# Performance work log

Hardware: AMD Instinct MI355X
Metric: run time of the kernel (lower is better)

## Reference

```python
import jax, jax.numpy as jnp
import numpy as np
from jax.scipy.special import logsumexp

B, DK, N, M = 16, 512, 1024, 1024
SINKHORN_ITERS = 5
EPS = 1e-8


def setup_inputs() -> dict:
    key = jax.random.key(0)
    k1, k2, k3, k4, k5 = jax.random.split(key, 5)
    return {
        "src_embedding": jax.random.normal(k1, (B, DK, N), dtype=jnp.float32),
        "tgt_embedding": jax.random.normal(k2, (B, DK, M), dtype=jnp.float32),
        "src": jax.random.normal(k3, (B, 3, N), dtype=jnp.float32),
        "tgt": jax.random.normal(k4, (B, 3, M), dtype=jnp.float32),
        # temperature must be positive; uniform in [0.05, 1.0)
        "temperature": jax.random.uniform(k5, (B,), dtype=jnp.float32, minval=0.05, maxval=1.0),
    }


def sinkhorn(scores, n_iters):
    # ZeroPad2d((0,1,0,1)): pad one slack row and one slack column with zeros
    scores = jnp.pad(scores, ((0, 0), (0, 1), (0, 1)))
    for _ in range(n_iters):
        # row normalization (all rows except slack row)
        top = scores[:, :-1, :] - logsumexp(scores[:, :-1, :], axis=2, keepdims=True)
        scores = jnp.concatenate([top, scores[:, -1:, :]], axis=1)
        # column normalization (all cols except slack col)
        left = scores[:, :, :-1] - logsumexp(scores[:, :, :-1], axis=1, keepdims=True)
        scores = jnp.concatenate([left, scores[:, :, -1:]], axis=2)
    return scores[:, :-1, :-1]


def reference(src_embedding, tgt_embedding, src, tgt, temperature):
    b, d_k, n = src_embedding.shape
    # [B, N, M] similarity scores
    dists = jnp.einsum('bdn,bdm->bnm', src_embedding, tgt_embedding) / jnp.sqrt(jnp.float32(d_k))
    affinity = dists / temperature[:, None, None]
    log_perm = sinkhorn(affinity, SINKHORN_ITERS)
    perm = jnp.exp(log_perm)                                             # [B,N,M]
    perm_norm = perm / (jnp.sum(perm, axis=2, keepdims=True) + EPS)      # [B,N,M]
    # soft correspondence: weighted_tgt[b,:,i] = sum_j perm_norm[b,i,j] * tgt[b,:,j]
    weighted_tgt = jnp.einsum('bdm,bnm->bdn', tgt, perm_norm)            # [B,3,N]
    weights = jnp.sum(perm, axis=-1, keepdims=True)                      # [B,N,1]
    weights_norm = weights / (jnp.sum(weights, axis=1, keepdims=True) + EPS)
    weights_norm = jnp.swapaxes(weights_norm, 1, 2)                      # [B,1,N]
    src_centroid = jnp.sum(src * weights_norm, axis=2, keepdims=True)    # [B,3,1]
    tgt_centroid = jnp.sum(weighted_tgt * weights_norm, axis=2, keepdims=True)
    src_centered = src - src_centroid
    corr_centered = (weighted_tgt - tgt_centroid) * weights_norm
    # weighted cross-covariance, batched 3x3
    H = jnp.einsum('bin,bjn->bij', src_centered, corr_centered)          # [B,3,3]
    # batched Procrustes via SVD (torch.svd: H = u diag(s) v^T; jnp: H = u diag(s) vh)
    u, s, vh = jnp.linalg.svd(H)
    v = jnp.swapaxes(vh, 1, 2)
    ut = jnp.swapaxes(u, 1, 2)
    r = jnp.matmul(v, ut)
    r_det = jnp.linalg.det(r)                                            # [B]
    diag = jnp.stack([jnp.ones_like(r_det), jnp.ones_like(r_det), r_det], axis=-1)  # [B,3]
    R = jnp.matmul(v * diag[:, None, :], ut)                             # [B,3,3]
    t = (jnp.matmul(-R, src_centroid) + tgt_centroid).reshape(b, 3)
    return R, t, perm_norm
```

## Files before the change

### kernel.cpp

```cpp
#include <hip/hip_runtime.h>
#include <math.h>

#define BB 16
#define NN 1024
#define MM 1024
#define DKK 512
#define RBLK 16
#define NRB  (NN/RBLK)

typedef short short8 __attribute__((ext_vector_type(8)));
typedef float f32x4 __attribute__((ext_vector_type(4)));

__device__ float g_u[BB*NN];
__device__ float g_v[BB*MM];
__device__ float g_w[BB*NN];
__device__ float g_wt[BB*3*NN];
__device__ float g_pm[BB*NRB*MM];
__device__ float g_ps[BB*NRB*MM];
__device__ __attribute__((aligned(16))) unsigned short gAh[BB*NN*DKK];
__device__ __attribute__((aligned(16))) unsigned short gAl[BB*NN*DKK];
__device__ __attribute__((aligned(16))) unsigned short gBh[BB*MM*DKK];
__device__ __attribute__((aligned(16))) unsigned short gBl[BB*MM*DKK];

__global__ __launch_bounds__(256) void zero_v_kernel() {
    int i = blockIdx.x*256 + threadIdx.x;
    if (i < BB*MM) g_v[i] = 0.0f;
}

__device__ __forceinline__ unsigned int bf16_rne(float x){
    unsigned int u = __float_as_uint(x);
    return (u + 0x7fffu + ((u>>16)&1u)) >> 16;
}

__global__ __launch_bounds__(256) void convert_split(const float* __restrict__ X,
                                                     int which) {
    unsigned short* Hh = which ? gBh : gAh;
    unsigned short* Hl = which ? gBl : gAl;
    int b  = blockIdx.z;
    int d0 = blockIdx.y * 64;
    int i0 = blockIdx.x * 64;
    __shared__ float T[64*65];
    const float* Xb = X + ((size_t)b*DKK + d0)*NN + i0;
    int t = threadIdx.x;
#pragma unroll
    for (int it=0; it<4; ++it){
        int lin = t + 256*it;
        int d = lin >> 4;
        int i4 = lin & 15;
        float4 v = *(const float4*)(Xb + (size_t)d*NN + i4*4);
        T[(i4*4+0)*65 + d] = v.x;
        T[(i4*4+1)*65 + d] = v.y;
        T[(i4*4+2)*65 + d] = v.z;
        T[(i4*4+3)*65 + d] = v.w;
    }
    __syncthreads();
    size_t obase = ((size_t)b*NN + i0)*DKK + d0;
#pragma unroll
    for (int it=0; it<2; ++it){
        int c = t + 256*it;
        int i = c >> 3;
        int p = c & 7;
        unsigned int hw[4], lw[4];
#pragma unroll
        for (int j=0;j<4;j++){
            float x0 = T[i*65 + p*8 + 2*j];
            float x1 = T[i*65 + p*8 + 2*j+1];
            unsigned int h0 = bf16_rne(x0);
            unsigned int h1 = bf16_rne(x1);
            float hf0 = __uint_as_float(h0<<16);
            float hf1 = __uint_as_float(h1<<16);
            unsigned int l0 = bf16_rne(x0 - hf0);
            unsigned int l1 = bf16_rne(x1 - hf1);
            hw[j] = h0 | (h1<<16);
            lw[j] = l0 | (l1<<16);
        }
        size_t eo = obase + (size_t)i*DKK + p*8;
        uint4 hv; hv.x=hw[0]; hv.y=hw[1]; hv.z=hw[2]; hv.w=hw[3];
        uint4 lv; lv.x=lw[0]; lv.y=lw[1]; lv.z=lw[2]; lv.w=lw[3];
        *(uint4*)(Hh + eo) = hv;
        *(uint4*)(Hl + eo) = lv;
    }
}

__global__ __launch_bounds__(256) void gemm_mfma(const float* __restrict__ temp,
                                                 float* __restrict__ C) {
    int id   = blockIdx.x;
    int xcd  = id & 7;
    int slot = id >> 3;
    int b    = xcd*2 + (slot >> 6);
    int sub  = slot & 63;
    int i0   = (sub >> 3) << 7;
    int j0   = (sub & 7) << 7;
    __shared__ __attribute__((aligned(16))) char lds[40960];
    int t = threadIdx.x;
    int lane = t & 63, w = t >> 6;
    int wr = w >> 1, wc = w & 1;
    const size_t eb = (size_t)b * NN * DKK;
    const uint4* pAh = (const uint4*)(gAh + eb);
    const uint4* pAl = (const uint4*)(gAl + eb);
    const uint4* pBh = (const uint4*)(gBh + eb);
    const uint4* pBl = (const uint4*)(gBl + eb);
    int rr = t >> 2, pp = t & 3;

    f32x4 acc[16];
#pragma unroll
    for (int q=0;q<16;q++) acc[q] = (f32x4){0.f,0.f,0.f,0.f};

    uint4 ra0, ra1, la0, la1, rb0, rb1, lb0, lb1;
    auto loadk = [&](int k0){
        int kq = k0 >> 3;
        ra0 = pAh[(size_t)(i0+rr)*64 + kq + pp];
        ra1 = pAh[(size_t)(i0+rr+64)*64 + kq + pp];
        la0 = pAl[(size_t)(i0+rr)*64 + kq + pp];
        la1 = pAl[(size_t)(i0+rr+64)*64 + kq + pp];
        rb0 = pBh[(size_t)(j0+rr)*64 + kq + pp];
        rb1 = pBh[(size_t)(j0+rr+64)*64 + kq + pp];
        lb0 = pBl[(size_t)(j0+rr)*64 + kq + pp];
        lb1 = pBl[(size_t)(j0+rr+64)*64 + kq + pp];
    };
    loadk(0);

    const char* fa = lds + (wr*64 + (lane&15))*80 + (lane>>4)*16;
    const char* fb = lds + 20480 + (wc*64 + (lane&15))*80 + (lane>>4)*16;
    char* wbase = lds + rr*80 + pp*16;

    for (int ks=0; ks<16; ++ks){
        __syncthreads();
        *(uint4*)(wbase + 0)     = ra0;
        *(uint4*)(wbase + 5120)  = ra1;
        *(uint4*)(wbase + 10240) = la0;
        *(uint4*)(wbase + 15360) = la1;
        *(uint4*)(wbase + 20480) = rb0;
        *(uint4*)(wbase + 25600) = rb1;
        *(uint4*)(wbase + 30720) = lb0;
        *(uint4*)(wbase + 35840) = lb1;
        __syncthreads();
        if (ks+1 < 16) loadk((ks+1)*32);

        short8 ah[4], al[4];
#pragma unroll
        for (int mf=0;mf<4;mf++){
            ah[mf] = *(const short8*)(fa + mf*1280);
            al[mf] = *(const short8*)(fa + 10240 + mf*1280);
        }
#pragma unroll
        for (int nf=0;nf<4;nf++){
            short8 bh = *(const short8*)(fb + nf*1280);
            short8 bl = *(const short8*)(fb + 10240 + nf*1280);
#pragma unroll
            for (int mf=0;mf<4;mf++){
                acc[mf*4+nf] = __builtin_amdgcn_mfma_f32_16x16x32_bf16(ah[mf], bh, acc[mf*4+nf], 0,0,0);
                acc[mf*4+nf] = __builtin_amdgcn_mfma_f32_16x16x32_bf16(ah[mf], bl, acc[mf*4+nf], 0,0,0);
                acc[mf*4+nf] = __builtin_amdgcn_mfma_f32_16x16x32_bf16(al[mf], bh, acc[mf*4+nf], 0,0,0);
            }
        }
    }

    float scale = 1.0f/(22.62741699796952f * temp[b]);
    float* Cb = C + ((size_t)b<<20);
    int r0c = i0 + wr*64 + ((lane>>4)<<2);
    int c0c = j0 + wc*64 + (lane&15);
#pragma unroll
    for (int mf=0;mf<4;mf++){
#pragma unroll
        for (int r2=0;r2<4;r2++){
            float* rowp = Cb + (size_t)(r0c + mf*16 + r2)*MM + c0c;
#pragma unroll
            for (int nf=0;nf<4;nf++)
                rowp[nf*16] = acc[mf*4+nf][r2]*scale;
        }
    }
}

__global__ __launch_bounds__(256) void sink_iter(const float* __restrict__ S) {
    int b   = blockIdx.y;
    int rb  = blockIdx.x;
    int row0 = rb*RBLK;
    int t = threadIdx.x;
    __shared__ float Ls[RBLK*1028];
    __shared__ float v_l[1024];
    __shared__ float u_l[RBLK];

    float4 v4 = *(const float4*)(g_v + (b<<10) + t*4);
    *(float4*)(v_l + t*4) = v4;

    const float* Sb = S + ((size_t)b*NN + row0)*MM;
#pragma unroll
    for (int rr=0; rr<RBLK; ++rr){
        float4 s4 = *(const float4*)(Sb + (size_t)rr*MM + t*4);
        s4.x -= v4.x; s4.y -= v4.y; s4.z -= v4.z; s4.w -= v4.w;
        *(float4*)(&Ls[rr*1028 + t*4]) = s4;
    }
    __syncthreads();

    {
        int r = t >> 4, c = t & 15;
        const float* Lr = &Ls[r*1028 + c];
        float m = -INFINITY;
#pragma unroll
        for (int k=0;k<64;k++) m = fmaxf(m, Lr[16*k]);
#pragma unroll
        for (int off=1; off<16; off<<=1) m = fmaxf(m, __shfl_xor(m, off));
        m = fmaxf(m, 0.0f);
        float s = 0.0f;
#pragma unroll
        for (int k=0;k<64;k++) s += __expf(Lr[16*k] - m);
#pragma unroll
        for (int off=1; off<16; off<<=1) s += __shfl_xor(s, off);
        s += __expf(-m);
        float u = m + __logf(s);
        if (c==0){ u_l[r] = u; g_u[b*NN + row0 + r] = u; }
    }
    __syncthreads();

    float mm[4], ss[4];
#pragma unroll
    for (int q=0;q<4;q++){ mm[q]=-INFINITY; ss[q]=0.f; }
#pragma unroll
    for (int r=0;r<RBLK;++r){
        float ur = u_l[r];
        const float* Lr = &Ls[r*1028];
#pragma unroll
        for (int q=0;q<4;q++)
            mm[q] = fmaxf(mm[q], Lr[t + 256*q] - ur);
    }
#pragma unroll
    for (int r=0;r<RBLK;++r){
        float ur = u_l[r];
        const float* Lr = &Ls[r*1028];
#pragma unroll
        for (int q=0;q<4;q++)
            ss[q] += __expf(Lr[t + 256*q] - ur - mm[q]);
    }
    size_t pbase = ((size_t)(b*NRB + rb) << 10) + t;
#pragma unroll
    for (int q=0;q<4;q++){
        g_pm[pbase + 256*q] = mm[q] + v_l[t + 256*q];
        g_ps[pbase + 256*q] = ss[q];
    }
}

__global__ __launch_bounds__(256) void col_lse_combine() {
    int idx = blockIdx.x*256 + threadIdx.x;
    int b = idx >> 10; int j = idx & (MM-1);
    float m = -INFINITY, s = 0.0f;
    size_t base = ((size_t)(b*NRB) << 10) + j;
    for (int c=0;c<NRB;c++){
        float om = g_pm[base + ((size_t)c<<10)];
        float os = g_ps[base + ((size_t)c<<10)];
        float nm = fmaxf(m, om);
        s = s*__expf(m-nm) + os*__expf(om-nm);
        m = nm;
    }
    float nm = fmaxf(m, 0.0f);
    s = s*__expf(m-nm) + __expf(-nm);
    g_v[idx] = nm + __logf(s);
}

__global__ __launch_bounds__(256) void finalize_rows(float* __restrict__ S,
                                                     const float* __restrict__ tgt) {
    int row  = blockIdx.x*4 + (threadIdx.x>>6);
    int lane = threadIdx.x & 63;
    int b = row >> 10;
    int i = row & (NN-1);
    float ui = g_u[row];
    float4* srow = (float4*)(S + (size_t)row*MM);
    const float4* vb = (const float4*)(g_v + (b<<10));
    const float4* t0 = (const float4*)(tgt + (size_t)b*3*MM);
    const float4* t1 = (const float4*)(tgt + (size_t)b*3*MM + MM);
    const float4* t2 = (const float4*)(tgt + (size_t)b*3*MM + 2*MM);
    float p[16];
    float rs=0.f, a0=0.f, a1=0.f, a2=0.f;
#pragma unroll
    for (int k=0;k<4;k++){
        float4 s4 = srow[lane + 64*k];
        float4 v4 = vb[lane + 64*k];
        p[4*k+0] = __expf(s4.x - ui - v4.x);
        p[4*k+1] = __expf(s4.y - ui - v4.y);
        p[4*k+2] = __expf(s4.z - ui - v4.z);
        p[4*k+3] = __expf(s4.w - ui - v4.w);
        rs += p[4*k+0]+p[4*k+1]+p[4*k+2]+p[4*k+3];
        float4 w0 = t0[lane + 64*k];
        float4 w1 = t1[lane + 64*k];
        float4 w2 = t2[lane + 64*k];
        a0 += p[4*k+0]*w0.x + p[4*k+1]*w0.y + p[4*k+2]*w0.z + p[4*k+3]*w0.w;
        a1 += p[4*k+0]*w1.x + p[4*k+1]*w1.y + p[4*k+2]*w1.z + p[4*k+3]*w1.w;
        a2 += p[4*k+0]*w2.x + p[4*k+1]*w2.y + p[4*k+2]*w2.z + p[4*k+3]*w2.w;
    }
    for (int off=32; off; off>>=1){
        rs += __shfl_xor(rs, off);
        a0 += __shfl_xor(a0, off);
        a1 += __shfl_xor(a1, off);
        a2 += __shfl_xor(a2, off);
    }
    float inv = 1.0f/(rs + 1e-8f);
#pragma unroll
    for (int k=0;k<4;k++){
        srow[lane + 64*k] = make_float4(p[4*k+0]*inv, p[4*k+1]*inv, p[4*k+2]*inv, p[4*k+3]*inv);
    }
    if (lane==0){
        g_w[row] = rs;
        g_wt[(b*3+0)*NN + i] = a0*inv;
        g_wt[(b*3+1)*NN + i] = a1*inv;
        g_wt[(b*3+2)*NN + i] = a2*inv;
    }
}

__global__ __launch_bounds__(256) void procrustes(const float* __restrict__ src,
                                                  float* __restrict__ out) {
    int b = blockIdx.x;
    int t = threadIdx.x;
    __shared__ float red[256];
    auto bsum = [&](float v)->float{
        red[t]=v; __syncthreads();
        for (int o=128;o>0;o>>=1){ if(t<o) red[t]+=red[t+o]; __syncthreads(); }
        float r=red[0]; __syncthreads(); return r;
    };
    const float* wrow = g_w + b*NN;
    float pw=0.f;
    for (int i=t;i<NN;i+=256) pw += wrow[i];
    float W = bsum(pw);
    float winv = 1.0f/(W + 1e-8f);
    const float* sb  = src  + (size_t)b*3*NN;
    const float* wtb = g_wt + (size_t)b*3*NN;
    float sc[3], tc[3];
    for (int c=0;c<3;c++){
        float p1=0.f,p2=0.f;
        for (int i=t;i<NN;i+=256){
            float wn = wrow[i]*winv;
            p1 += sb[c*NN+i]*wn;
            p2 += wtb[c*NN+i]*wn;
        }
        sc[c]=bsum(p1);
        tc[c]=bsum(p2);
    }
    float H[9];
    for (int c=0;c<3;c++)
        for (int d=0;d<3;d++){
            float p=0.f;
            for (int i=t;i<NN;i+=256){
                float wn = wrow[i]*winv;
                p += (sb[c*NN+i]-sc[c]) * ((wtb[d*NN+i]-tc[d])*wn);
            }
            H[c*3+d]=bsum(p);
        }
    if (t==0){
        double Hd[3][3];
        for (int r2=0;r2<3;r2++) for (int c2=0;c2<3;c2++) Hd[r2][c2]=H[r2*3+c2];
        double K[3][3];
        for (int i2=0;i2<3;i2++)
            for (int j2=0;j2<3;j2++){
                double acc=0;
                for (int r2=0;r2<3;r2++) acc += Hd[r2][i2]*Hd[r2][j2];
                K[i2][j2]=acc;
            }
        double V[3][3]={{1,0,0},{0,1,0},{0,0,1}};
        const int PQ[3][2]={{0,1},{0,2},{1,2}};
        for (int sweep=0; sweep<30; ++sweep){
            double off = fabs(K[0][1])+fabs(K[0][2])+fabs(K[1][2]);
            if (off < 1e-26) break;
            for (int pi=0; pi<3; ++pi){
                int p = PQ[pi][0], q = PQ[pi][1];
                double apq = K[p][q];
                if (fabs(apq) < 1e-300) continue;
                double tau = (K[q][q]-K[p][p])/(2.0*apq);
                double tt  = (tau>=0.0?1.0:-1.0)/(fabs(tau)+sqrt(1.0+tau*tau));
                double c   = 1.0/sqrt(1.0+tt*tt);
                double s   = tt*c;
                double Kpp=K[p][p], Kqq=K[q][q];
                K[p][p] = Kpp - tt*apq;
                K[q][q] = Kqq + tt*apq;
                K[p][q] = 0.0; K[q][p] = 0.0;
                int r2 = 3-p-q;
                double Krp=K[r2][p], Krq=K[r2][q];
                K[r2][p] = c*Krp - s*Krq; K[p][r2]=K[r2][p];
                K[r2][q] = s*Krp + c*Krq; K[q][r2]=K[r2][q];
                for (int rr=0; rr<3; ++rr){
                    double vp=V[rr][p], vq=V[rr][q];
                    V[rr][p] = c*vp - s*vq;
                    V[rr][q] = s*vp + c*vq;
                }
            }
        }
        double lam[3]={K[0][0],K[1][1],K[2][2]};
        int o0=0,o1=1,o2=2,tmp;
        if (lam[o0]<lam[o1]){tmp=o0;o0=o1;o1=tmp;}
        if (lam[o0]<lam[o2]){tmp=o0;o0=o2;o2=tmp;}
        if (lam[o1]<lam[o2]){tmp=o1;o1=o2;o2=tmp;}
        int ord[3]={o0,o1,o2};
        double Vs[3][3], U[3][3];
        for (int k=0;k<3;k++)
            for (int r2=0;r2<3;r2++) Vs[r2][k]=V[r2][ord[k]];
        for (int k=0;k<3;k++){
            double ux = Hd[0][0]*Vs[0][k] + Hd[0][1]*Vs[1][k] + Hd[0][2]*Vs[2][k];
            double uy = Hd[1][0]*Vs[0][k] + Hd[1][1]*Vs[1][k] + Hd[1][2]*Vs[2][k];
            double uz = Hd[2][0]*Vs[0][k] + Hd[2][1]*Vs[1][k] + Hd[2][2]*Vs[2][k];
            double n = sqrt(ux*ux+uy*uy+uz*uz);
            if (n > 1e-30){ U[0][k]=ux/n; U[1][k]=uy/n; U[2][k]=uz/n; }
            else {
                double cx = U[1][0]*U[2][1]-U[2][0]*U[1][1];
                double cy = U[2][0]*U[0][1]-U[0][0]*U[2][1];
                double cz = U[0][0]*U[1][1]-U[1][0]*U[0][1];
                U[0][k]=cx; U[1][k]=cy; U[2][k]=cz;
            }
        }
        double rm[3][3];
        for (int i2=0;i2<3;i2++)
            for (int j2=0;j2<3;j2++)
                rm[i2][j2] = Vs[i2][0]*U[j2][0] + Vs[i2][1]*U[j2][1] + Vs[i2][2]*U[j2][2];
        double det = rm[0][0]*(rm[1][1]*rm[2][2]-rm[1][2]*rm[2][1])
                   - rm[0][1]*(rm[1][0]*rm[2][2]-rm[1][2]*rm[2][0])
                   + rm[0][2]*(rm[1][0]*rm[2][1]-rm[1][1]*rm[2][0]);
        double R[3][3];
        for (int i2=0;i2<3;i2++)
            for (int j2=0;j2<3;j2++)
                R[i2][j2] = Vs[i2][0]*U[j2][0] + Vs[i2][1]*U[j2][1] + det*Vs[i2][2]*U[j2][2];
        double tv[3];
        for (int i2=0;i2<3;i2++)
            tv[i2] = -(R[i2][0]*sc[0]+R[i2][1]*sc[1]+R[i2][2]*sc[2]) + tc[i2];
        for (int i2=0;i2<3;i2++)
            for (int j2=0;j2<3;j2++)
                out[b*9 + i2*3 + j2] = (float)R[i2][j2];
        for (int i2=0;i2<3;i2++)
            out[144 + b*3 + i2] = (float)tv[i2];
    }
}

extern "C" void kernel_launch(void* const* d_in, const int* in_sizes, int n_in,
                              void* d_out, int out_size, void* d_ws, size_t ws_size,
                              hipStream_t stream) {
    const float* src_emb = (const float*)d_in[0];
    const float* tgt_emb = (const float*)d_in[1];
    const float* src     = (const float*)d_in[2];
    const float* tgt     = (const float*)d_in[3];
    const float* temp    = (const float*)d_in[4];
    float* out = (float*)d_out;
    float* S = out + 192;

    hipLaunchKernelGGL(zero_v_kernel, dim3(64), dim3(256), 0, stream);
    hipLaunchKernelGGL(convert_split, dim3(16,8,16), dim3(256), 0, stream, src_emb, 0);
    hipLaunchKernelGGL(convert_split, dim3(16,8,16), dim3(256), 0, stream, tgt_emb, 1);
    hipLaunchKernelGGL(gemm_mfma, dim3(1024), dim3(256), 0, stream, temp, S);
    for (int it=0; it<5; ++it){
        hipLaunchKernelGGL(sink_iter, dim3(NRB,BB), dim3(256), 0, stream, S);
        hipLaunchKernelGGL(col_lse_combine, dim3(64), dim3(256), 0, stream);
    }
    hipLaunchKernelGGL(finalize_rows, dim3(4096), dim3(256), 0, stream, S, tgt);
    hipLaunchKernelGGL(procrustes, dim3(16), dim3(256), 0, stream, src, out);
}
```

Before: 366.1 us.

## Use direct global-to-LDS loads with double buffering and swizzled layout in split-bf16 GEMM

The GEMM main loop now uses global_load_lds to copy the hi/lo bf16 tiles straight into a double-buffered 64KB LDS region. This removes the register staging, the padded-row stores and one barrier per k-step. The conversion kernel writes a swizzled k-chunk order so the unpadded LDS reads avoid bank conflicts, and the two conversion launches are merged into one grid. The MFMA loop is reordered into three passes over hi/lo fragments, which lowers register pressure. The larger LDS footprint may reduce occupancy, and the swizzle must match exactly between producer and consumer.

```diff
diff --git a/kernel.cpp b/kernel.cpp
--- a/kernel.cpp
+++ b/kernel.cpp
@@ -32,11 +32,20 @@
     return (u + 0x7fffu + ((u>>16)&1u)) >> 16;
 }
 
-__global__ __launch_bounds__(256) void convert_split(const float* __restrict__ X,
-                                                     int which) {
+__device__ __forceinline__ void gl_lds(const void* g, void* l){
+    __builtin_amdgcn_global_load_lds(
+        (const __attribute__((address_space(1))) unsigned int*)g,
+        (__attribute__((address_space(3))) unsigned int*)l, 16, 0, 0);
+}
+
+__global__ __launch_bounds__(256) void convert_split(const float* __restrict__ A,
+                                                     const float* __restrict__ Bm) {
+    int z = blockIdx.z;
+    int which = z >> 4;
+    int b = z & 15;
+    const float* X = which ? Bm : A;
     unsigned short* Hh = which ? gBh : gAh;
     unsigned short* Hl = which ? gBl : gAl;
-    int b  = blockIdx.z;
     int d0 = blockIdx.y * 64;
     int i0 = blockIdx.x * 64;
     __shared__ float T[64*65];
@@ -74,7 +83,8 @@
             hw[j] = h0 | (h1<<16);
             lw[j] = l0 | (l1<<16);
         }
-        size_t eo = obase + (size_t)i*DKK + p*8;
+        int pw = (p & 4) | ((p + (i>>1)) & 3);
+        size_t eo = obase + (size_t)i*DKK + pw*8;
         uint4 hv; hv.x=hw[0]; hv.y=hw[1]; hv.z=hw[2]; hv.w=hw[3];
         uint4 lv; lv.x=lw[0]; lv.y=lw[1]; lv.z=lw[2]; lv.w=lw[3];
         *(uint4*)(Hh + eo) = hv;
@@ -91,69 +101,85 @@
     int sub  = slot & 63;
     int i0   = (sub >> 3) << 7;
     int j0   = (sub & 7) << 7;
-    __shared__ __attribute__((aligned(16))) char lds[40960];
+    __shared__ __attribute__((aligned(16))) char lds[65536];
     int t = threadIdx.x;
     int lane = t & 63, w = t >> 6;
     int wr = w >> 1, wc = w & 1;
-    const size_t eb = (size_t)b * NN * DKK;
-    const uint4* pAh = (const uint4*)(gAh + eb);
-    const uint4* pAl = (const uint4*)(gAl + eb);
-    const uint4* pBh = (const uint4*)(gBh + eb);
-    const uint4* pBl = (const uint4*)(gBl + eb);
-    int rr = t >> 2, pp = t & 3;
+    const size_t ebytes = (size_t)b * NN * DKK * 2;
+
+    const char* src[8];
+    int dstoff[8];
+    {
+        int rql = lane >> 2, cl = lane & 3;
+#pragma unroll
+        for (int o=0;o<4;o++){
+            const char* g = (o==0) ? (const char*)gAh : (o==1) ? (const char*)gAl
+                           : (o==2) ? (const char*)gBh : (const char*)gBl;
+            int t0 = (o<2) ? i0 : j0;
+#pragma unroll
+            for (int q=0;q<2;q++){
+                int rloc = w*32 + q*16 + rql;
+                src[o*2+q] = g + ebytes + (size_t)(t0 + rloc)*1024 + cl*16;
+                dstoff[o*2+q] = o*8192 + (w*32 + q*16)*64;
+            }
+        }
+    }
 
     f32x4 acc[16];
 #pragma unroll
     for (int q=0;q<16;q++) acc[q] = (f32x4){0.f,0.f,0.f,0.f};
 
-    uint4 ra0, ra1, la0, la1, rb0, rb1, lb0, lb1;
-    auto loadk = [&](int k0){
-        int kq = k0 >> 3;
-        ra0 = pAh[(size_t)(i0+rr)*64 + kq + pp];
-        ra1 = pAh[(size_t)(i0+rr+64)*64 + kq + pp];
-        la0 = pAl[(size_t)(i0+rr)*64 + kq + pp];
-        la1 = pAl[(size_t)(i0+rr+64)*64 + kq + pp];
-        rb0 = pBh[(size_t)(j0+rr)*64 + kq + pp];
-        rb1 = pBh[(size_t)(j0+rr+64)*64 + kq + pp];
-        lb0 = pBl[(size_t)(j0+rr)*64 + kq + pp];
-        lb1 = pBl[(size_t)(j0+rr+64)*64 + kq + pp];
-    };
-    loadk(0);
-
-    const char* fa = lds + (wr*64 + (lane&15))*80 + (lane>>4)*16;
-    const char* fb = lds + 20480 + (wc*64 + (lane&15))*80 + (lane>>4)*16;
-    char* wbase = lds + rr*80 + pp*16;
+    int fslot = ((lane>>4) + ((lane&15)>>1)) & 3;
+    int arow = wr*64 + (lane&15);
+    int brow = wc*64 + (lane&15);
+    int faoff = arow*64 + fslot*16;
+    int fboff = 16384 + brow*64 + fslot*16;
+
+#pragma unroll
+    for (int idx=0;idx<8;idx++) gl_lds(src[idx], lds + dstoff[idx]);
 
     for (int ks=0; ks<16; ++ks){
         __syncthreads();
-        *(uint4*)(wbase + 0)     = ra0;
-        *(uint4*)(wbase + 5120)  = ra1;
-        *(uint4*)(wbase + 10240) = la0;
-        *(uint4*)(wbase + 15360) = la1;
-        *(uint4*)(wbase + 20480) = rb0;
-        *(uint4*)(wbase + 25600) = rb1;
-        *(uint4*)(wbase + 30720) = lb0;
-        *(uint4*)(wbase + 35840) = lb1;
-        __syncthreads();
-        if (ks+1 < 16) loadk((ks+1)*32);
-
-        short8 ah[4], al[4];
-#pragma unroll
-        for (int mf=0;mf<4;mf++){
-            ah[mf] = *(const short8*)(fa + mf*1280);
-            al[mf] = *(const short8*)(fa + 10240 + mf*1280);
-        }
-#pragma unroll
-        for (int nf=0;nf<4;nf++){
-            short8 bh = *(const short8*)(fb + nf*1280);
-            short8 bl = *(const short8*)(fb + 10240 + nf*1280);
-#pragma unroll
-            for (int mf=0;mf<4;mf++){
-                acc[mf*4+nf] = __builtin_amdgcn_mfma_f32_16x16x32_bf16(ah[mf], bh, acc[mf*4+nf], 0,0,0);
-                acc[mf*4+nf] = __builtin_amdgcn_mfma_f32_16x16x32_bf16(ah[mf], bl, acc[mf*4+nf], 0,0,0);
-                acc[mf*4+nf] = __builtin_amdgcn_mfma_f32_16x16x32_bf16(al[mf], bh, acc[mf*4+nf], 0,0,0);
-            }
-        }
+        int cur = (ks & 1) * 32768;
+        if (ks+1 < 16){
+            int nxt = ((ks+1) & 1) * 32768;
+#pragma unroll
+            for (int idx=0;idx<8;idx++){
+                src[idx] += 64;
+                gl_lds(src[idx], lds + nxt + dstoff[idx]);
+            }
+        }
+        const char* fa = lds + cur + faoff;
+        const char* fb = lds + cur + fboff;
+
+        short8 ah[4], bh[4];
+#pragma unroll
+        for (int mf=0;mf<4;mf++) ah[mf] = *(const short8*)(fa + mf*1024);
+#pragma unroll
+        for (int nf=0;nf<4;nf++) bh[nf] = *(const short8*)(fb + nf*1024);
+#pragma unroll
+        for (int nf=0;nf<4;nf++)
+#pragma unroll
+            for (int mf=0;mf<4;mf++)
+                acc[mf*4+nf] = __builtin_amdgcn_mfma_f32_16x16x32_bf16(ah[mf], bh[nf], acc[mf*4+nf], 0,0,0);
+
+        short8 al[4];
+#pragma unroll
+        for (int mf=0;mf<4;mf++) al[mf] = *(const short8*)(fa + 8192 + mf*1024);
+#pragma unroll
+        for (int nf=0;nf<4;nf++)
+#pragma unroll
+            for (int mf=0;mf<4;mf++)
+                acc[mf*4+nf] = __builtin_amdgcn_mfma_f32_16x16x32_bf16(al[mf], bh[nf], acc[mf*4+nf], 0,0,0);
+
+        short8 bl[4];
+#pragma unroll
+        for (int nf=0;nf<4;nf++) bl[nf] = *(const short8*)(fb + 8192 + nf*1024);
+#pragma unroll
+        for (int nf=0;nf<4;nf++)
+#pragma unroll
+            for (int mf=0;mf<4;mf++)
+                acc[mf*4+nf] = __builtin_amdgcn_mfma_f32_16x16x32_bf16(ah[mf], bl[nf], acc[mf*4+nf], 0,0,0);
     }
 
     float scale = 1.0f/(22.62741699796952f * temp[b]);
@@ -438,8 +464,7 @@
     float* S = out + 192;
 
     hipLaunchKernelGGL(zero_v_kernel, dim3(64), dim3(256), 0, stream);
-    hipLaunchKernelGGL(convert_split, dim3(16,8,16), dim3(256), 0, stream, src_emb, 0);
-    hipLaunchKernelGGL(convert_split, dim3(16,8,16), dim3(256), 0, stream, tgt_emb, 1);
+    hipLaunchKernelGGL(convert_split, dim3(16,8,32), dim3(256), 0, stream, src_emb, tgt_emb);
     hipLaunchKernelGGL(gemm_mfma, dim3(1024), dim3(256), 0, stream, temp, S);
     for (int it=0; it<5; ++it){
         hipLaunchKernelGGL(sink_iter, dim3(NRB,BB), dim3(256), 0, stream, S);
```

Measured after the change: 360.1 us. No clear change (-1.6%).
